# Performance work log

Measured on AMD Instinct MI355X. Metric: run time of the kernel, lower is better.

## Reference

```python
import jax, jax.numpy as jnp
import numpy as np


def _apply_ry(state, theta, i, n):
    # state: [B, 2^n] complex; theta: scalar or [B]
    B = state.shape[0]
    s = state.reshape(B, 2**i, 2, 2**(n - i - 1))
    th = jnp.reshape(theta, (-1, 1, 1)) * 0.5
    c, sn = jnp.cos(th), jnp.sin(th)
    a0, a1 = s[:, :, 0], s[:, :, 1]
    return jnp.stack([c * a0 - sn * a1, sn * a0 + c * a1], axis=2).reshape(B, -1)


def _apply_rz(state, theta, i, n):
    B = state.shape[0]
    s = state.reshape(B, 2**i, 2, 2**(n - i - 1))
    ph = jnp.exp(-0.5j * jnp.reshape(theta, (-1, 1, 1)).astype(jnp.float32))
    return jnp.stack([s[:, :, 0] * ph, s[:, :, 1] * jnp.conj(ph)], axis=2).reshape(B, -1)


def _apply_cnot(state, c, t, n):
    # CNOT(control=c, target=t); flips target amplitudes on control=1 slice
    B = state.shape[0]
    s = state.reshape((B,) + (2,) * n)
    ax_c, ax_t = 1 + c, 1 + t
    zero = jnp.take(s, 0, axis=ax_c)
    one = jnp.take(s, 1, axis=ax_c)
    one = jnp.flip(one, axis=ax_t - (1 if t > c else 0))
    return jnp.stack([zero, one], axis=ax_c).reshape(B, -1)


def _z_signs(n):
    # signs[i, k] = +1 if bit i of basis index k is 0 else -1 (qubit 0 = MSB)
    idx = np.arange(2**n)
    bits = (idx[None, :] >> (n - 1 - np.arange(n))[:, None]) & 1
    return jnp.asarray(1.0 - 2.0 * bits, dtype=jnp.float32)  # [n, 2^n]


def _circuit(q_in, w_ry, w_rz):
    # Batched state-vector simulation of: AngleEmbedding(RY) ->
    # n_layers x (per-qubit RY,RZ + CNOT ring) -> <Z_i> expectations.
    B, n = q_in.shape
    L = w_ry.shape[0]
    state = jnp.zeros((B, 2**n), jnp.complex64).at[:, 0].set(1.0)
    for i in range(n):  # AngleEmbedding with rotation='Y'
        state = _apply_ry(state, q_in[:, i], i, n)
    for l in range(L):
        for i in range(n):
            state = _apply_ry(state, w_ry[l, i], i, n)
            state = _apply_rz(state, w_rz[l, i], i, n)
        for i in range(n):  # CNOT ring
            state = _apply_cnot(state, i, (i + 1) % n, n)
    probs = jnp.abs(state) ** 2  # [B, 2^n]
    return probs @ _z_signs(n).T  # [B, n] = <Z_i>


def setup_inputs():
    key = jax.random.key(0)
    ks = jax.random.split(key, 6)
    B, D, n, L = 4096, 512, 10, 4
    return {
        "x": jax.random.normal(ks[0], (B, D), jnp.float32),
        "pre_w": jax.random.normal(ks[1], (n, D), jnp.float32) / np.sqrt(D).astype(np.float32),
        "pre_b": jnp.zeros((n,), jnp.float32),
        "post_w": jax.random.normal(ks[2], (1, n), jnp.float32) / np.sqrt(n).astype(np.float32),
        "post_b": jnp.zeros((1,), jnp.float32),
        "w_ry": jax.random.normal(ks[3], (L, n), jnp.float32),
        "w_rz": jax.random.normal(ks[4], (L, n), jnp.float32),
    }


def reference(x, pre_w, pre_b, post_w, post_b, w_ry, w_rz):
    q_in = x @ pre_w.T + pre_b      # pre_net: [B, n_qubits] rotation angles
    z = _circuit(q_in, w_ry, w_rz)  # [B, n_qubits] PauliZ expectations
    return z @ post_w.T + post_b    # post_net: [B, 1] logits
```

## Files before the change

### kernel.cpp

```cpp
#include <hip/hip_runtime.h>

#define DEV static __device__ __forceinline__

template <int CTRL>
DEV float dpp_xor(float v) {
    int i = __float_as_int(v);
    i = __builtin_amdgcn_update_dpp(i, i, CTRL, 0xF, 0xF, false);
    return __int_as_float(i);
}
template <int PAT>
DEV float swz(float v) {
    return __int_as_float(__builtin_amdgcn_ds_swizzle(__float_as_int(v), PAT));
}
DEV float bperm(int byteaddr, float v) {
    return __int_as_float(__builtin_amdgcn_ds_bpermute(byteaddr, __float_as_int(v)));
}

template <int MASK>
DEV float lanexor(float v, int a32) {
    if constexpr (MASK == 1)       return dpp_xor<0xB1>(v);
    else if constexpr (MASK == 2)  return dpp_xor<0x4E>(v);
    else if constexpr (MASK == 8)  return dpp_xor<0x128>(v);
    else if constexpr (MASK == 4)  return swz<0x101F>(v);
    else if constexpr (MASK == 16) return swz<0x401F>(v);
    else                           return bperm(a32, v);
}

DEV float wave_sum(float v, int a32) {
    v += lanexor<1>(v, 0);
    v += lanexor<2>(v, 0);
    v += lanexor<4>(v, 0);
    v += lanexor<8>(v, 0);
    v += lanexor<16>(v, 0);
    v += bperm(a32, v);
    return v;
}


template <int P>
DEV void apply_ry(float (&re)[16], float (&im)[16], float c, float s, int lane, int a32) {
    if constexpr (P >= 4) {
        constexpr int mask = 1 << (P - 4);
        const float sg = (lane & mask) ? s : -s;
#pragma unroll
        for (int r = 0; r < 16; ++r) {
            float pr = lanexor<mask>(re[r], a32);
            float pi = lanexor<mask>(im[r], a32);
            re[r] = fmaf(c, re[r], sg * pr);
            im[r] = fmaf(c, im[r], sg * pi);
        }
    } else {
        constexpr int tb = 1 << P;
#pragma unroll
        for (int r = 0; r < 16; ++r) {
            if (!(r & tb)) {
                const int r2 = r | tb;
                float a0r = re[r], a1r = re[r2];
                float a0i = im[r], a1i = im[r2];
                re[r]  = fmaf(c, a0r, -s * a1r);
                re[r2] = fmaf(s, a0r,  c * a1r);
                im[r]  = fmaf(c, a0i, -s * a1i);
                im[r2] = fmaf(s, a0i,  c * a1i);
            }
        }
    }
}

DEV int g_of(int a) {
    a ^= ((a >> 1) & 1) ? 1 : 0;
    a ^= ((a >> 2) & 1) ? 2 : 0;
    a ^= ((a >> 3) & 1) ? 4 : 0;
    a ^= ((a >> 4) & 1) ? 8 : 0;
    a ^= ((a >> 5) & 1) ? 16 : 0;
    return a;
}

__global__ void dqc_trig_kernel(const float* __restrict__ w_ry,
                                const float* __restrict__ w_rz,
                                float2* __restrict__ trig) {
    int t = threadIdx.x;
    if (t < 80) {
        float ang = (t < 40 ? w_ry[t] : w_rz[t - 40]) * 0.5f;
        trig[t] = make_float2(__cosf(ang), __sinf(ang));
    }
}

__global__ __launch_bounds__(256, 4) void dqc_main_kernel(
    const float* __restrict__ x, const float* __restrict__ pre_w,
    const float* __restrict__ pre_b, const float* __restrict__ post_w,
    const float* __restrict__ post_b, const float2* __restrict__ trig,
    float* __restrict__ out, int B) {
    const int lane = threadIdx.x & 63;
    const int wid = threadIdx.x >> 6;
    const int b = blockIdx.x * 4 + wid;
    if (b >= B) return;

    const int a32 = (lane ^ 32) << 2;
    const int h0 = lane ^ ((lane & 1) ? 32 : 0);
    const int cA = g_of(h0) << 2;
    const int cB = g_of(h0 ^ 32) << 2;

    float th[10];
#pragma unroll
    for (int i = 0; i < 10; ++i) th[i] = 0.f;
    const float* xb = x + (size_t)b * 512;
#pragma unroll
    for (int k = 0; k < 8; ++k) {
        const int idx = lane + 64 * k;
        float xv = xb[idx];
#pragma unroll
        for (int i = 0; i < 10; ++i) th[i] = fmaf(xv, pre_w[i * 512 + idx], th[i]);
    }
#pragma unroll
    for (int i = 0; i < 10; ++i) th[i] = wave_sum(th[i], a32) + pre_b[i];

    float cc[10], ss[10];
#pragma unroll
    for (int i = 0; i < 10; ++i) {
        float a = th[i] * 0.5f;
        cc[i] = __cosf(a);
        ss[i] = __sinf(a);
    }
    float laneP = 1.f;
#pragma unroll
    for (int i = 0; i < 6; ++i)
        laneP *= ((lane >> (5 - i)) & 1) ? ss[i] : cc[i];
    float hi4[4], lo4[4];
#pragma unroll
    for (int j = 0; j < 4; ++j) {
        float f6 = (j >> 1) ? ss[6] : cc[6];
        float f7 = (j & 1) ? ss[7] : cc[7];
        hi4[j] = laneP * f6 * f7;
        float f8 = (j >> 1) ? ss[8] : cc[8];
        float f9 = (j & 1) ? ss[9] : cc[9];
        lo4[j] = f8 * f9;
    }
    float re[16], im[16];
#pragma unroll
    for (int r = 0; r < 16; ++r) { re[r] = hi4[r >> 2] * lo4[r & 3]; im[r] = 0.f; }

#pragma unroll 1
    for (int l = 0; l < 4; ++l) {
        const float2* tr = trig + l * 10;
        const float2* tz = trig + 40 + l * 10;

        apply_ry<9>(re, im, tr[0].x, tr[0].y, lane, a32);
        apply_ry<8>(re, im, tr[1].x, tr[1].y, lane, a32);
        apply_ry<7>(re, im, tr[2].x, tr[2].y, lane, a32);
        apply_ry<6>(re, im, tr[3].x, tr[3].y, lane, a32);
        apply_ry<5>(re, im, tr[4].x, tr[4].y, lane, a32);
        apply_ry<4>(re, im, tr[5].x, tr[5].y, lane, a32);
        apply_ry<3>(re, im, tr[6].x, tr[6].y, lane, a32);
        apply_ry<2>(re, im, tr[7].x, tr[7].y, lane, a32);
        apply_ry<1>(re, im, tr[8].x, tr[8].y, lane, a32);
        apply_ry<0>(re, im, tr[9].x, tr[9].y, lane, a32);

        float plr, pli;
        {
            float2 z0 = tz[0];
            pli = ((lane >> 5) & 1) ? z0.y : -z0.y;
            plr = z0.x;
#pragma unroll
            for (int q = 1; q < 6; ++q) {
                float2 z = tz[q];
                float sq = ((lane >> (5 - q)) & 1) ? z.y : -z.y;
                float nr = plr * z.x - pli * sq;
                float ni = plr * sq + pli * z.x;
                plr = nr; pli = ni;
            }
        }
        float p67r[4], p67i[4], p89r[4], p89i[4];
        {
            const float c6 = tz[6].x, s6 = tz[6].y, c7 = tz[7].x, s7 = tz[7].y;
            const float c8 = tz[8].x, s8 = tz[8].y, c9 = tz[9].x, s9 = tz[9].y;
#pragma unroll
            for (int j = 0; j < 4; ++j) {
                float sg6 = (j >> 1) ? s6 : -s6;
                float sg7 = (j & 1) ? s7 : -s7;
                float ar = c6 * c7 - sg6 * sg7;
                float ai = c6 * sg7 + sg6 * c7;
                p67r[j] = ar * plr - ai * pli;
                p67i[j] = ar * pli + ai * plr;
                float sg8 = (j >> 1) ? s8 : -s8;
                float sg9 = (j & 1) ? s9 : -s9;
                p89r[j] = c8 * c9 - sg8 * sg9;
                p89i[j] = c8 * sg9 + sg8 * c9;
            }
        }
#pragma unroll
        for (int r = 0; r < 16; ++r) {
            const int j = r >> 2, k = r & 3;
            float t_r = re[r] * p67r[j] - im[r] * p67i[j];
            float t_i = re[r] * p67i[j] + im[r] * p67r[j];
            re[r] = t_r * p89r[k] - t_i * p89i[k];
            im[r] = t_r * p89i[k] + t_i * p89r[k];
        }

#pragma unroll
        for (int r = 0; r < 16; ++r) {
            const int addr = ((0x6996 >> r) & 1) ? cB : cA;
            re[r] = bperm(addr, re[r]);
            im[r] = bperm(addr, im[r]);
        }
        {
            const bool ctrl = (lane & 1) != 0;
#pragma unroll
            for (int r = 0; r < 8; ++r) {
                const int r2 = r | 8;
                float t0 = re[r], t1 = re[r2];
                re[r]  = ctrl ? t1 : t0;
                re[r2] = ctrl ? t0 : t1;
                float u0 = im[r], u1 = im[r2];
                im[r]  = ctrl ? u1 : u0;
                im[r2] = ctrl ? u0 : u1;
            }
        }
#pragma unroll
        for (int r = 0; r < 16; ++r)
            if ((r & 8) && !(r & 4)) {
                const int r2 = r | 4;
                float t = re[r]; re[r] = re[r2]; re[r2] = t;
                t = im[r]; im[r] = im[r2]; im[r2] = t;
            }
#pragma unroll
        for (int r = 0; r < 16; ++r)
            if ((r & 4) && !(r & 2)) {
                const int r2 = r | 2;
                float t = re[r]; re[r] = re[r2]; re[r2] = t;
                t = im[r]; im[r] = im[r2]; im[r2] = t;
            }
#pragma unroll
        for (int r = 0; r < 16; ++r)
            if ((r & 2) && !(r & 1)) {
                const int r2 = r | 1;
                float t = re[r]; re[r] = re[r2]; re[r2] = t;
                t = im[r]; im[r] = im[r2]; im[r2] = t;
            }
    }

    float laneC = 0.f;
#pragma unroll
    for (int j = 0; j < 6; ++j) {
        int bit = (lane >> (5 - j)) & 1;
        laneC += post_w[j] * (1.f - 2.f * (float)bit);
    }
    float acc = 0.f;
#pragma unroll
    for (int r = 0; r < 16; ++r) {
        float regC = 0.f;
#pragma unroll
        for (int j = 6; j < 10; ++j) {
            int bit = (r >> (9 - j)) & 1;
            regC += post_w[j] * (1.f - 2.f * (float)bit);
        }
        float p = fmaf(re[r], re[r], im[r] * im[r]);
        acc = fmaf(p, laneC + regC, acc);
    }
    acc = wave_sum(acc, a32);
    if (lane == 0) out[b] = acc + post_b[0];
}

extern "C" void kernel_launch(void* const* d_in, const int* in_sizes, int n_in,
                              void* d_out, int out_size, void* d_ws, size_t ws_size,
                              hipStream_t stream) {
    const float* x      = (const float*)d_in[0];
    const float* pre_w  = (const float*)d_in[1];
    const float* pre_b  = (const float*)d_in[2];
    const float* post_w = (const float*)d_in[3];
    const float* post_b = (const float*)d_in[4];
    const float* w_ry   = (const float*)d_in[5];
    const float* w_rz   = (const float*)d_in[6];
    float* out = (float*)d_out;
    float2* trig = (float2*)d_ws;

    const int B = in_sizes[0] / 512;

    dqc_trig_kernel<<<1, 128, 0, stream>>>(w_ry, w_rz, trig);
    dqc_main_kernel<<<(B + 3) / 4, 256, 0, stream>>>(x, pre_w, pre_b, post_w,
                                                     post_b, trig, out, B);
}
```

Measured before the change: 100.5 us.

## Process two batch samples per wavefront with interleaved state vectors

Each wavefront now simulates two batch elements at once, keeping two 32-register complex state vectors, and applies every gate and lane shuffle to both. The extra independent work is meant to hide shuffle and permute latency and to amortize the pre_w loads, which now use float4 vector loads shared between the two samples. Register pressure roughly doubles, so the launch bounds drop to 2 blocks per CU. The grid shrinks accordingly, which lowers occupancy and can leave fewer waves to hide latency.

```diff
diff --git a/kernel.cpp b/kernel.cpp
--- a/kernel.cpp
+++ b/kernel.cpp
@@ -25,6 +25,10 @@
     else if constexpr (MASK == 16) return swz<0x401F>(v);
     else                           return bperm(a32, v);
 }
+template <int MASK>
+DEV float2 lanexor2(float2 v, int a32) {
+    return make_float2(lanexor<MASK>(v.x, a32), lanexor<MASK>(v.y, a32));
+}
 
 DEV float wave_sum(float v, int a32) {
     v += lanexor<1>(v, 0);
@@ -36,18 +40,24 @@
     return v;
 }
 
+DEV float2 cmul(float2 a, float2 b) {
+    return make_float2(a.x * b.x - a.y * b.y, a.x * b.y + a.y * b.x);
+}
+
 
 template <int P>
-DEV void apply_ry(float (&re)[16], float (&im)[16], float c, float s, int lane, int a32) {
+DEV void ry2(float2 (&A)[16], float2 (&B)[16], float c, float s, int lane, int a32) {
     if constexpr (P >= 4) {
         constexpr int mask = 1 << (P - 4);
         const float sg = (lane & mask) ? s : -s;
 #pragma unroll
         for (int r = 0; r < 16; ++r) {
-            float pr = lanexor<mask>(re[r], a32);
-            float pi = lanexor<mask>(im[r], a32);
-            re[r] = fmaf(c, re[r], sg * pr);
-            im[r] = fmaf(c, im[r], sg * pi);
+            float2 pa = lanexor2<mask>(A[r], a32);
+            float2 pb = lanexor2<mask>(B[r], a32);
+            A[r].x = fmaf(c, A[r].x, sg * pa.x);
+            A[r].y = fmaf(c, A[r].y, sg * pa.y);
+            B[r].x = fmaf(c, B[r].x, sg * pb.x);
+            B[r].y = fmaf(c, B[r].y, sg * pb.y);
         }
     } else {
         constexpr int tb = 1 << P;
@@ -55,12 +65,12 @@
         for (int r = 0; r < 16; ++r) {
             if (!(r & tb)) {
                 const int r2 = r | tb;
-                float a0r = re[r], a1r = re[r2];
-                float a0i = im[r], a1i = im[r2];
-                re[r]  = fmaf(c, a0r, -s * a1r);
-                re[r2] = fmaf(s, a0r,  c * a1r);
-                im[r]  = fmaf(c, a0i, -s * a1i);
-                im[r2] = fmaf(s, a0i,  c * a1i);
+                float2 a0 = A[r], a1 = A[r2];
+                A[r]  = make_float2(fmaf(c, a0.x, -s * a1.x), fmaf(c, a0.y, -s * a1.y));
+                A[r2] = make_float2(fmaf(s, a0.x,  c * a1.x), fmaf(s, a0.y,  c * a1.y));
+                float2 b0 = B[r], b1 = B[r2];
+                B[r]  = make_float2(fmaf(c, b0.x, -s * b1.x), fmaf(c, b0.y, -s * b1.y));
+                B[r2] = make_float2(fmaf(s, b0.x,  c * b1.x), fmaf(s, b0.y,  c * b1.y));
             }
         }
     }
@@ -85,91 +95,111 @@
     }
 }
 
-__global__ __launch_bounds__(256, 4) void dqc_main_kernel(
+__global__ __launch_bounds__(256, 2) void dqc_main_kernel(
     const float* __restrict__ x, const float* __restrict__ pre_w,
     const float* __restrict__ pre_b, const float* __restrict__ post_w,
     const float* __restrict__ post_b, const float2* __restrict__ trig,
     float* __restrict__ out, int B) {
     const int lane = threadIdx.x & 63;
     const int wid = threadIdx.x >> 6;
-    const int b = blockIdx.x * 4 + wid;
-    if (b >= B) return;
+    const int w = blockIdx.x * 4 + wid;
+    const int b0 = w * 2, b1 = w * 2 + 1;
+    if (b0 >= B) return;
+    const int b1c = (b1 < B) ? b1 : b0;
 
     const int a32 = (lane ^ 32) << 2;
     const int h0 = lane ^ ((lane & 1) ? 32 : 0);
     const int cA = g_of(h0) << 2;
     const int cB = g_of(h0 ^ 32) << 2;
 
-    float th[10];
-#pragma unroll
-    for (int i = 0; i < 10; ++i) th[i] = 0.f;
-    const float* xb = x + (size_t)b * 512;
-#pragma unroll
-    for (int k = 0; k < 8; ++k) {
-        const int idx = lane + 64 * k;
-        float xv = xb[idx];
-#pragma unroll
-        for (int i = 0; i < 10; ++i) th[i] = fmaf(xv, pre_w[i * 512 + idx], th[i]);
-    }
-#pragma unroll
-    for (int i = 0; i < 10; ++i) th[i] = wave_sum(th[i], a32) + pre_b[i];
-
-    float cc[10], ss[10];
+    float thA[10], thB[10];
+#pragma unroll
+    for (int i = 0; i < 10; ++i) { thA[i] = 0.f; thB[i] = 0.f; }
+    const float4* xa4 = (const float4*)(x + (size_t)b0 * 512);
+    const float4* xb4 = (const float4*)(x + (size_t)b1c * 512);
+#pragma unroll
+    for (int k = 0; k < 2; ++k) {
+        const int vi = lane + 64 * k;
+        float4 xva = xa4[vi];
+        float4 xvb = xb4[vi];
+#pragma unroll
+        for (int i = 0; i < 10; ++i) {
+            float4 wv = ((const float4*)(pre_w + i * 512))[vi];
+            thA[i] = fmaf(xva.x, wv.x, thA[i]);
+            thB[i] = fmaf(xvb.x, wv.x, thB[i]);
+            thA[i] = fmaf(xva.y, wv.y, thA[i]);
+            thB[i] = fmaf(xvb.y, wv.y, thB[i]);
+            thA[i] = fmaf(xva.z, wv.z, thA[i]);
+            thB[i] = fmaf(xvb.z, wv.z, thB[i]);
+            thA[i] = fmaf(xva.w, wv.w, thA[i]);
+            thB[i] = fmaf(xvb.w, wv.w, thB[i]);
+        }
+    }
 #pragma unroll
     for (int i = 0; i < 10; ++i) {
-        float a = th[i] * 0.5f;
-        cc[i] = __cosf(a);
-        ss[i] = __sinf(a);
-    }
-    float laneP = 1.f;
-#pragma unroll
-    for (int i = 0; i < 6; ++i)
-        laneP *= ((lane >> (5 - i)) & 1) ? ss[i] : cc[i];
-    float hi4[4], lo4[4];
-#pragma unroll
-    for (int j = 0; j < 4; ++j) {
-        float f6 = (j >> 1) ? ss[6] : cc[6];
-        float f7 = (j & 1) ? ss[7] : cc[7];
-        hi4[j] = laneP * f6 * f7;
-        float f8 = (j >> 1) ? ss[8] : cc[8];
-        float f9 = (j & 1) ? ss[9] : cc[9];
-        lo4[j] = f8 * f9;
-    }
-    float re[16], im[16];
-#pragma unroll
-    for (int r = 0; r < 16; ++r) { re[r] = hi4[r >> 2] * lo4[r & 3]; im[r] = 0.f; }
+        thA[i] = wave_sum(thA[i], a32) + pre_b[i];
+        thB[i] = wave_sum(thB[i], a32) + pre_b[i];
+    }
+
+    float2 A[16], Bst[16];
+    {
+        float ccA[10], ssA[10], ccB[10], ssB[10];
+#pragma unroll
+        for (int i = 0; i < 10; ++i) {
+            float aa = thA[i] * 0.5f, ab = thB[i] * 0.5f;
+            ccA[i] = __cosf(aa); ssA[i] = __sinf(aa);
+            ccB[i] = __cosf(ab); ssB[i] = __sinf(ab);
+        }
+        float lpA = 1.f, lpB = 1.f;
+#pragma unroll
+        for (int i = 0; i < 6; ++i) {
+            const int bit = (lane >> (5 - i)) & 1;
+            lpA *= bit ? ssA[i] : ccA[i];
+            lpB *= bit ? ssB[i] : ccB[i];
+        }
+        float hiA[4], loA[4], hiB[4], loB[4];
+#pragma unroll
+        for (int j = 0; j < 4; ++j) {
+            hiA[j] = lpA * ((j >> 1) ? ssA[6] : ccA[6]) * ((j & 1) ? ssA[7] : ccA[7]);
+            loA[j] = ((j >> 1) ? ssA[8] : ccA[8]) * ((j & 1) ? ssA[9] : ccA[9]);
+            hiB[j] = lpB * ((j >> 1) ? ssB[6] : ccB[6]) * ((j & 1) ? ssB[7] : ccB[7]);
+            loB[j] = ((j >> 1) ? ssB[8] : ccB[8]) * ((j & 1) ? ssB[9] : ccB[9]);
+        }
+#pragma unroll
+        for (int r = 0; r < 16; ++r) {
+            A[r]   = make_float2(hiA[r >> 2] * loA[r & 3], 0.f);
+            Bst[r] = make_float2(hiB[r >> 2] * loB[r & 3], 0.f);
+        }
+    }
 
 #pragma unroll 1
     for (int l = 0; l < 4; ++l) {
         const float2* tr = trig + l * 10;
         const float2* tz = trig + 40 + l * 10;
 
-        apply_ry<9>(re, im, tr[0].x, tr[0].y, lane, a32);
-        apply_ry<8>(re, im, tr[1].x, tr[1].y, lane, a32);
-        apply_ry<7>(re, im, tr[2].x, tr[2].y, lane, a32);
-        apply_ry<6>(re, im, tr[3].x, tr[3].y, lane, a32);
-        apply_ry<5>(re, im, tr[4].x, tr[4].y, lane, a32);
-        apply_ry<4>(re, im, tr[5].x, tr[5].y, lane, a32);
-        apply_ry<3>(re, im, tr[6].x, tr[6].y, lane, a32);
-        apply_ry<2>(re, im, tr[7].x, tr[7].y, lane, a32);
-        apply_ry<1>(re, im, tr[8].x, tr[8].y, lane, a32);
-        apply_ry<0>(re, im, tr[9].x, tr[9].y, lane, a32);
-
-        float plr, pli;
+        ry2<9>(A, Bst, tr[0].x, tr[0].y, lane, a32);
+        ry2<8>(A, Bst, tr[1].x, tr[1].y, lane, a32);
+        ry2<7>(A, Bst, tr[2].x, tr[2].y, lane, a32);
+        ry2<6>(A, Bst, tr[3].x, tr[3].y, lane, a32);
+        ry2<5>(A, Bst, tr[4].x, tr[4].y, lane, a32);
+        ry2<4>(A, Bst, tr[5].x, tr[5].y, lane, a32);
+        ry2<3>(A, Bst, tr[6].x, tr[6].y, lane, a32);
+        ry2<2>(A, Bst, tr[7].x, tr[7].y, lane, a32);
+        ry2<1>(A, Bst, tr[8].x, tr[8].y, lane, a32);
+        ry2<0>(A, Bst, tr[9].x, tr[9].y, lane, a32);
+
+        float2 pl;
         {
             float2 z0 = tz[0];
-            pli = ((lane >> 5) & 1) ? z0.y : -z0.y;
-            plr = z0.x;
+            pl = make_float2(z0.x, ((lane >> 5) & 1) ? z0.y : -z0.y);
 #pragma unroll
             for (int q = 1; q < 6; ++q) {
                 float2 z = tz[q];
                 float sq = ((lane >> (5 - q)) & 1) ? z.y : -z.y;
-                float nr = plr * z.x - pli * sq;
-                float ni = plr * sq + pli * z.x;
-                plr = nr; pli = ni;
-            }
-        }
-        float p67r[4], p67i[4], p89r[4], p89i[4];
+                pl = cmul(pl, make_float2(z.x, sq));
+            }
+        }
+        float2 p67[4], p89[4];
         {
             const float c6 = tz[6].x, s6 = tz[6].y, c7 = tz[7].x, s7 = tz[7].y;
             const float c8 = tz[8].x, s8 = tz[8].y, c9 = tz[9].x, s9 = tz[9].y;
@@ -177,64 +207,60 @@
             for (int j = 0; j < 4; ++j) {
                 float sg6 = (j >> 1) ? s6 : -s6;
                 float sg7 = (j & 1) ? s7 : -s7;
-                float ar = c6 * c7 - sg6 * sg7;
-                float ai = c6 * sg7 + sg6 * c7;
-                p67r[j] = ar * plr - ai * pli;
-                p67i[j] = ar * pli + ai * plr;
+                p67[j] = cmul(cmul(make_float2(c6, sg6), make_float2(c7, sg7)), pl);
                 float sg8 = (j >> 1) ? s8 : -s8;
                 float sg9 = (j & 1) ? s9 : -s9;
-                p89r[j] = c8 * c9 - sg8 * sg9;
-                p89i[j] = c8 * sg9 + sg8 * c9;
+                p89[j] = cmul(make_float2(c8, sg8), make_float2(c9, sg9));
             }
         }
 #pragma unroll
         for (int r = 0; r < 16; ++r) {
             const int j = r >> 2, k = r & 3;
-            float t_r = re[r] * p67r[j] - im[r] * p67i[j];
-            float t_i = re[r] * p67i[j] + im[r] * p67r[j];
-            re[r] = t_r * p89r[k] - t_i * p89i[k];
-            im[r] = t_r * p89i[k] + t_i * p89r[k];
+            A[r]   = cmul(cmul(A[r], p67[j]), p89[k]);
+            Bst[r] = cmul(cmul(Bst[r], p67[j]), p89[k]);
         }
 
 #pragma unroll
         for (int r = 0; r < 16; ++r) {
             const int addr = ((0x6996 >> r) & 1) ? cB : cA;
-            re[r] = bperm(addr, re[r]);
-            im[r] = bperm(addr, im[r]);
+            A[r].x = bperm(addr, A[r].x);
+            A[r].y = bperm(addr, A[r].y);
+            Bst[r].x = bperm(addr, Bst[r].x);
+            Bst[r].y = bperm(addr, Bst[r].y);
         }
         {
             const bool ctrl = (lane & 1) != 0;
 #pragma unroll
             for (int r = 0; r < 8; ++r) {
                 const int r2 = r | 8;
-                float t0 = re[r], t1 = re[r2];
-                re[r]  = ctrl ? t1 : t0;
-                re[r2] = ctrl ? t0 : t1;
-                float u0 = im[r], u1 = im[r2];
-                im[r]  = ctrl ? u1 : u0;
-                im[r2] = ctrl ? u0 : u1;
+                float2 t0 = A[r], t1 = A[r2];
+                A[r]  = ctrl ? t1 : t0;
+                A[r2] = ctrl ? t0 : t1;
+                float2 u0 = Bst[r], u1 = Bst[r2];
+                Bst[r]  = ctrl ? u1 : u0;
+                Bst[r2] = ctrl ? u0 : u1;
             }
         }
 #pragma unroll
         for (int r = 0; r < 16; ++r)
             if ((r & 8) && !(r & 4)) {
                 const int r2 = r | 4;
-                float t = re[r]; re[r] = re[r2]; re[r2] = t;
-                t = im[r]; im[r] = im[r2]; im[r2] = t;
+                float2 t = A[r]; A[r] = A[r2]; A[r2] = t;
+                t = Bst[r]; Bst[r] = Bst[r2]; Bst[r2] = t;
             }
 #pragma unroll
         for (int r = 0; r < 16; ++r)
             if ((r & 4) && !(r & 2)) {
                 const int r2 = r | 2;
-                float t = re[r]; re[r] = re[r2]; re[r2] = t;
-                t = im[r]; im[r] = im[r2]; im[r2] = t;
+                float2 t = A[r]; A[r] = A[r2]; A[r2] = t;
+                t = Bst[r]; Bst[r] = Bst[r2]; Bst[r2] = t;
             }
 #pragma unroll
         for (int r = 0; r < 16; ++r)
             if ((r & 2) && !(r & 1)) {
                 const int r2 = r | 1;
-                float t = re[r]; re[r] = re[r2]; re[r2] = t;
-                t = im[r]; im[r] = im[r2]; im[r2] = t;
+                float2 t = A[r]; A[r] = A[r2]; A[r2] = t;
+                t = Bst[r]; Bst[r] = Bst[r2]; Bst[r2] = t;
             }
     }
 
@@ -244,7 +270,7 @@
         int bit = (lane >> (5 - j)) & 1;
         laneC += post_w[j] * (1.f - 2.f * (float)bit);
     }
-    float acc = 0.f;
+    float accA = 0.f, accB = 0.f;
 #pragma unroll
     for (int r = 0; r < 16; ++r) {
         float regC = 0.f;
@@ -253,11 +279,16 @@
             int bit = (r >> (9 - j)) & 1;
             regC += post_w[j] * (1.f - 2.f * (float)bit);
         }
-        float p = fmaf(re[r], re[r], im[r] * im[r]);
-        acc = fmaf(p, laneC + regC, acc);
-    }
-    acc = wave_sum(acc, a32);
-    if (lane == 0) out[b] = acc + post_b[0];
+        const float coef = laneC + regC;
+        accA = fmaf(fmaf(A[r].x, A[r].x, A[r].y * A[r].y), coef, accA);
+        accB = fmaf(fmaf(Bst[r].x, Bst[r].x, Bst[r].y * Bst[r].y), coef, accB);
+    }
+    accA = wave_sum(accA, a32);
+    accB = wave_sum(accB, a32);
+    if (lane == 0) {
+        out[b0] = accA + post_b[0];
+        if (b1 < B) out[b1] = accB + post_b[0];
+    }
 }
 
 extern "C" void kernel_launch(void* const* d_in, const int* in_sizes, int n_in,
@@ -276,6 +307,7 @@
     const int B = in_sizes[0] / 512;
 
     dqc_trig_kernel<<<1, 128, 0, stream>>>(w_ry, w_rz, trig);
-    dqc_main_kernel<<<(B + 3) / 4, 256, 0, stream>>>(x, pre_w, pre_b, post_w,
-                                                     post_b, trig, out, B);
-}
+    const int blocks = (B + 7) / 8;
+    dqc_main_kernel<<<blocks, 256, 0, stream>>>(x, pre_w, pre_b, post_w,
+                                                post_b, trig, out, B);
+}
```

New measurement: 102.7 us. +2.2%, slower.
